# Kernel tuning notes

Hardware: AMD Instinct MI355X
Metric: run time of the kernel (lower is better)

The kernel has to match this reference:

```python
import jax, jax.numpy as jnp
import numpy as np
import math

DIM = 2048
NUM_HEADS = 16
NUM_KV_HEADS = 4
HEAD_DIM = DIM // NUM_HEADS  # 128
KV_DIM = DIM * NUM_KV_HEADS // NUM_HEADS  # 512
B, T = 4, 2048


def setup_inputs() -> dict:
    key = jax.random.key(0)
    ks = jax.random.split(key, 12)
    s = 0.02
    return {
        "x": jax.random.normal(ks[0], (B, T, DIM), dtype=jnp.float32),
        "cos": jax.random.uniform(ks[1], (T, HEAD_DIM // 2), dtype=jnp.float32),
        "sin": jax.random.uniform(ks[2], (T, HEAD_DIM // 2), dtype=jnp.float32),
        "Wq": jax.random.normal(ks[3], (DIM, DIM), dtype=jnp.float32) * s,
        "bq": jnp.zeros((DIM,), dtype=jnp.float32),
        "Wk": jax.random.normal(ks[4], (DIM, KV_DIM), dtype=jnp.float32) * s,
        "bk": jnp.zeros((KV_DIM,), dtype=jnp.float32),
        "Wv": jax.random.normal(ks[5], (DIM, KV_DIM), dtype=jnp.float32) * s,
        "bv": jnp.zeros((KV_DIM,), dtype=jnp.float32),
        "Wo": jax.random.normal(ks[6], (DIM, DIM), dtype=jnp.float32) * s,
        "bo": jnp.zeros((DIM,), dtype=jnp.float32),
    }


def _rope(t, cos, sin):
    # t: [B, H, T, D]; cos/sin: [T, D/2] broadcast over (B, H)
    t1, t2 = t[..., ::2], t[..., 1::2]
    return jnp.concatenate([t1 * cos - t2 * sin, t1 * sin + t2 * cos], axis=-1)


def reference(x, cos, sin, Wq, bq, Wk, bk, Wv, bv, Wo, bo):
    Bx, Tx, C = x.shape
    q = (x @ Wq + bq).reshape(Bx, Tx, NUM_HEADS, HEAD_DIM).transpose(0, 2, 1, 3)
    k = (x @ Wk + bk).reshape(Bx, Tx, NUM_KV_HEADS, HEAD_DIM).transpose(0, 2, 1, 3)
    v = (x @ Wv + bv).reshape(Bx, Tx, NUM_KV_HEADS, HEAD_DIM).transpose(0, 2, 1, 3)
    rep = NUM_HEADS // NUM_KV_HEADS
    k = jnp.repeat(k, rep, axis=1)
    v = jnp.repeat(v, rep, axis=1)
    q = _rope(q, cos, sin)
    k = _rope(k, cos, sin)
    scores = jnp.einsum("bhqd,bhkd->bhqk", q, k) / math.sqrt(HEAD_DIM)
    attn = jax.nn.softmax(scores, axis=-1)
    out = jnp.einsum("bhqk,bhkd->bhqd", attn, v)
    out = out.transpose(0, 2, 1, 3).reshape(Bx, Tx, C)
    return out @ Wo + bo
```

## Files before the change

kernel.cpp:

```cpp
#include <hip/hip_runtime.h>

typedef unsigned short u16;
using bf16x8 = __attribute__((ext_vector_type(8))) short;
using u16x8  = __attribute__((ext_vector_type(8))) unsigned short;
using f32x4  = __attribute__((ext_vector_type(4))) float;
using u32x2  = __attribute__((ext_vector_type(2))) unsigned int;

__device__ __forceinline__ u16 f2bf(float f) {
  unsigned u = __float_as_uint(f);
  u += 0x7FFFu + ((u >> 16) & 1u);
  return (u16)(u >> 16);
}

__device__ __forceinline__ void gload_lds16(const void* g, void* l) {
  __builtin_amdgcn_global_load_lds(
      (const __attribute__((address_space(1))) unsigned int*)g,
      (__attribute__((address_space(3))) unsigned int*)l, 16, 0, 0);
}

__global__ __launch_bounds__(256) void k_cvt(const float* __restrict__ src,
                                             u16* __restrict__ dst) {
  size_t i = (size_t)blockIdx.x * 256 + threadIdx.x;
  const float4* s4 = (const float4*)src;
  float4 a = s4[i * 2], b = s4[i * 2 + 1];
  u16x8 r;
  r[0] = f2bf(a.x); r[1] = f2bf(a.y); r[2] = f2bf(a.z); r[3] = f2bf(a.w);
  r[4] = f2bf(b.x); r[5] = f2bf(b.y); r[6] = f2bf(b.z); r[7] = f2bf(b.w);
  *(u16x8*)(dst + i * 8) = r;
}

__global__ void k_transpose_cvt(const float* __restrict__ src, u16* __restrict__ dst,
                                int R, int C) {
  __shared__ float tile[32][33];
  int bx = blockIdx.x * 32, by = blockIdx.y * 32;
  int tx = threadIdx.x, ty = threadIdx.y;
#pragma unroll
  for (int j = 0; j < 4; ++j)
    tile[ty + j * 8][tx] = src[(size_t)(by + ty + j * 8) * C + bx + tx];
  __syncthreads();
#pragma unroll
  for (int j = 0; j < 4; ++j)
    dst[(size_t)(bx + ty + j * 8) * R + by + tx] = f2bf(tile[tx][ty + j * 8]);
}

__device__ __forceinline__ void gemm_core128(const u16* __restrict__ A,
                                             const u16* __restrict__ Bt, int K,
                                             int m0, int n0, u16* As, u16* Bs,
                                             f32x4 acc[4][4]) {
  const int tid  = threadIdx.x;
  const int lane = tid & 63;
  const int w    = tid >> 6;
  const int wr   = (w >> 1) * 64;
  const int wc   = (w & 1) * 64;
  const int srow = (w << 3) + (lane >> 3);
  const int scol = (lane & 7) << 3;
  const int lm   = lane & 15;
  const int lk   = (lane >> 4) << 3;

  for (int kt = 0; kt < K; kt += 64) {
#pragma unroll
    for (int i = 0; i < 4; ++i) {
      int r = (i << 5) + srow;
      gload_lds16(A  + (size_t)(m0 + r) * K + kt + scol, As + ((i * 4 + w) << 9));
      gload_lds16(Bt + (size_t)(n0 + r) * K + kt + scol, Bs + ((i * 4 + w) << 9));
    }
    __syncthreads();
#pragma unroll
    for (int kk = 0; kk < 64; kk += 32) {
      bf16x8 af[4], bfr[4];
#pragma unroll
      for (int m = 0; m < 4; ++m)
        af[m] = *(const bf16x8*)(As + (wr + m * 16 + lm) * 64 + kk + lk);
#pragma unroll
      for (int n = 0; n < 4; ++n)
        bfr[n] = *(const bf16x8*)(Bs + (wc + n * 16 + lm) * 64 + kk + lk);
#pragma unroll
      for (int m = 0; m < 4; ++m)
#pragma unroll
        for (int n = 0; n < 4; ++n)
          acc[m][n] = __builtin_amdgcn_mfma_f32_16x16x32_bf16(af[m], bfr[n], acc[m][n], 0, 0, 0);
    }
    __syncthreads();
  }
}

__global__ __launch_bounds__(256, 2) void k_qkv(
    const u16* __restrict__ xb, const u16* __restrict__ wT,
    const float* __restrict__ bq, const float* __restrict__ bk, const float* __restrict__ bv,
    const float* __restrict__ cosb, const float* __restrict__ sinb,
    u16* __restrict__ qbuf, u16* __restrict__ kbuf, u16* __restrict__ vbufT) {
  __shared__ u16 As[128 * 64], Bs[128 * 64];
  const int mt = blockIdx.x, nt = blockIdx.y;
  f32x4 acc[4][4];
#pragma unroll
  for (int m = 0; m < 4; ++m)
#pragma unroll
    for (int n = 0; n < 4; ++n) { f32x4 z = {0.f, 0.f, 0.f, 0.f}; acc[m][n] = z; }
  gemm_core128(xb, wT, 2048, mt * 128, nt * 128, As, Bs, acc);

  const int lane = threadIdx.x & 63, w = threadIdx.x >> 6;
  const int row0 = mt * 128 + (w >> 1) * 64 + ((lane >> 4) << 2);
  const int col0 = nt * 128 + (w & 1) * 64 + (lane & 15);
  const float qscale = 0.12751744f;

#pragma unroll
  for (int m = 0; m < 4; ++m) {
#pragma unroll
    for (int n = 0; n < 4; ++n) {
      const int gc = col0 + n * 16;
#pragma unroll
      for (int i = 0; i < 4; ++i) {
        const int gr = row0 + m * 16 + i;
        const int b = gr >> 11, t = gr & 2047;
        float v = acc[m][n][i];
        if (nt < 16) {
          int h = gc >> 7, d = gc & 127;
          float val = v + bq[gc];
          float part = __shfl_xor(val, 1);
          int ir = d >> 1;
          float c = cosb[t * 64 + ir], s = sinb[t * 64 + ir];
          float outv; int dd;
          if (d & 1) { outv = part * s + val * c; dd = ir + 64; }
          else       { outv = val * c - part * s; dd = ir; }
          qbuf[(((size_t)(b * 16 + h) * 2048 + t) << 7) + dd] = f2bf(outv * qscale);
        } else if (nt < 20) {
          int g2 = gc - 2048;
          int kvh = g2 >> 7, d = g2 & 127;
          float val = v + bk[g2];
          float part = __shfl_xor(val, 1);
          int ir = d >> 1;
          float c = cosb[t * 64 + ir], s = sinb[t * 64 + ir];
          float outv; int dd;
          if (d & 1) { outv = part * s + val * c; dd = ir + 64; }
          else       { outv = val * c - part * s; dd = ir; }
          kbuf[(((size_t)(b * 4 + kvh) * 2048 + t) << 7) + dd] = f2bf(outv);
        } else {
          int g2 = gc - 2560;
          int kvh = g2 >> 7, d = g2 & 127;
          float val = v + bv[g2];
          vbufT[((size_t)((b * 4 + kvh) * 128 + d)) * 2048 + t] = f2bf(val);
        }
      }
    }
  }
}

__global__ __launch_bounds__(128, 2) void k_attn(const u16* __restrict__ qbuf,
                                                 const u16* __restrict__ kbuf,
                                                 const u16* __restrict__ vbufT,
                                                 u16* __restrict__ ob) {
  __shared__ u16 Ks[64 * 128];
  __shared__ u16 Vs[128 * 64];
  __shared__ u16 Ps[64 * 64];

  const int f = blockIdx.x;
  const int x = f & 7, mm = f >> 3;
  const int g = x * 2 + (mm >> 7);
  const int mem = mm & 127;
  const int b = g >> 2, kvh = g & 3;
  const int h = kvh * 4 + (mem >> 5);
  const int qt = mem & 31;

  const int tid = threadIdx.x, lane = tid & 63, w = tid >> 6;
  const int lm = lane & 15, lg = lane >> 4;

  const u16* qb = qbuf + ((size_t)((b * 16 + h) * 2048 + qt * 64)) * 128;
  const u16* kb = kbuf + ((size_t)(b * 4 + kvh) * 2048) * 128;
  const u16* vb = vbufT + ((size_t)(b * 4 + kvh) * 128) * 2048;

  bf16x8 qf[2][4];
#pragma unroll
  for (int st = 0; st < 2; ++st)
#pragma unroll
    for (int dc = 0; dc < 4; ++dc)
      qf[st][dc] = *(const bf16x8*)(qb + (size_t)(w * 32 + st * 16 + lm) * 128 + dc * 32 + (lg << 3));

  f32x4 o[2][8];
#pragma unroll
  for (int st = 0; st < 2; ++st)
#pragma unroll
    for (int dn = 0; dn < 8; ++dn) { f32x4 z = {0.f, 0.f, 0.f, 0.f}; o[st][dn] = z; }
  float lsum[2] = {0.f, 0.f};

  for (int kt = 0; kt < 2048; kt += 64) {
#pragma unroll
    for (int j = 0; j < 8; ++j) {
      int seg = j * 2 + w;
      int cK = seg * 64 + lane;
      int rK = cK >> 4, ccK = cK & 15;
      gload_lds16(kb + (size_t)(kt + rK) * 128 + ((ccK ^ (rK & 7)) << 3), Ks + (seg << 9));
      int dV = seg * 8 + (lane >> 3), ccV = lane & 7;
      gload_lds16(vb + (size_t)dV * 2048 + kt + ((ccV ^ (dV & 7)) << 3), Vs + (seg << 9));
    }
    __syncthreads();

#pragma unroll
    for (int kg = 0; kg < 4; ++kg) {
      const int krow = kg * 16 + lm;
      bf16x8 kf[4];
#pragma unroll
      for (int dc = 0; dc < 4; ++dc)
        kf[dc] = *(const bf16x8*)(Ks + krow * 128 + (((dc * 4 + lg) ^ (krow & 7)) << 3));
      f32x4 s0 = {0.f, 0.f, 0.f, 0.f}, s1 = {0.f, 0.f, 0.f, 0.f};
#pragma unroll
      for (int dc = 0; dc < 4; ++dc) {
        s0 = __builtin_amdgcn_mfma_f32_16x16x32_bf16(kf[dc], qf[0][dc], s0, 0, 0, 0);
        s1 = __builtin_amdgcn_mfma_f32_16x16x32_bf16(kf[dc], qf[1][dc], s1, 0, 0, 0);
      }
#pragma unroll
      for (int st = 0; st < 2; ++st) {
        f32x4 sv = st ? s1 : s0;
        float p0 = __builtin_amdgcn_exp2f(sv[0]);
        float p1 = __builtin_amdgcn_exp2f(sv[1]);
        float p2 = __builtin_amdgcn_exp2f(sv[2]);
        float p3 = __builtin_amdgcn_exp2f(sv[3]);
        lsum[st] += (p0 + p1) + (p2 + p3);
        unsigned lo = (unsigned)f2bf(p0) | ((unsigned)f2bf(p1) << 16);
        unsigned hi = (unsigned)f2bf(p2) | ((unsigned)f2bf(p3) << 16);
        const int q = w * 32 + st * 16 + lm;
        const int chunk = kg * 2 + (lg >> 1);
        u16* dst = Ps + q * 64 + ((chunk ^ (q & 7)) << 3) + ((lg & 1) << 2);
        u32x2 pk; pk[0] = lo; pk[1] = hi;
        *reinterpret_cast<u32x2*>(dst) = pk;
      }
    }

#pragma unroll
    for (int kstep = 0; kstep < 2; ++kstep) {
      bf16x8 pf[2];
#pragma unroll
      for (int st = 0; st < 2; ++st) {
        const int q = w * 32 + st * 16 + lm;
        pf[st] = *(const bf16x8*)(Ps + q * 64 + (((kstep * 4 + lg) ^ (q & 7)) << 3));
      }
#pragma unroll
      for (int dn = 0; dn < 8; ++dn) {
        const int d = dn * 16 + lm;
        bf16x8 vf = *(const bf16x8*)(Vs + d * 64 + (((kstep * 4 + lg) ^ (d & 7)) << 3));
        o[0][dn] = __builtin_amdgcn_mfma_f32_16x16x32_bf16(pf[0], vf, o[0][dn], 0, 0, 0);
        o[1][dn] = __builtin_amdgcn_mfma_f32_16x16x32_bf16(pf[1], vf, o[1][dn], 0, 0, 0);
      }
    }
    __syncthreads();
  }

#pragma unroll
  for (int st = 0; st < 2; ++st) {
    float L = lsum[st];
    L += __shfl_xor(L, 16);
    L += __shfl_xor(L, 32);
#pragma unroll
    for (int i = 0; i < 4; ++i) {
      float inv = 1.0f / __shfl(L, lg * 4 + i);
      int t = qt * 64 + w * 32 + st * 16 + lg * 4 + i;
#pragma unroll
      for (int dn = 0; dn < 8; ++dn) {
        int d = dn * 16 + lm;
        ob[((size_t)(b * 2048 + t)) * 2048 + h * 128 + d] = f2bf(o[st][dn][i] * inv);
      }
    }
  }
}

__global__ __launch_bounds__(256, 2) void k_oproj(const u16* __restrict__ ab,
                                                  const u16* __restrict__ woT,
                                                  const float* __restrict__ bo,
                                                  float* __restrict__ out) {
  __shared__ u16 As[128 * 64], Bs[128 * 64];
  const int mt = blockIdx.x, nt = blockIdx.y;
  f32x4 acc[4][4];
#pragma unroll
  for (int m = 0; m < 4; ++m)
#pragma unroll
    for (int n = 0; n < 4; ++n) { f32x4 z = {0.f, 0.f, 0.f, 0.f}; acc[m][n] = z; }
  gemm_core128(ab, woT, 2048, mt * 128, nt * 128, As, Bs, acc);

  const int lane = threadIdx.x & 63, w = threadIdx.x >> 6;
  const int row0 = mt * 128 + (w >> 1) * 64 + ((lane >> 4) << 2);
  const int col0 = nt * 128 + (w & 1) * 64 + (lane & 15);
#pragma unroll
  for (int m = 0; m < 4; ++m)
#pragma unroll
    for (int n = 0; n < 4; ++n) {
      const int gc = col0 + n * 16;
      const float bias = bo[gc];
#pragma unroll
      for (int i = 0; i < 4; ++i) {
        const int gr = row0 + m * 16 + i;
        out[(size_t)gr * 2048 + gc] = acc[m][n][i] + bias;
      }
    }
}

extern "C" void kernel_launch(void* const* d_in, const int* in_sizes, int n_in,
                              void* d_out, int out_size, void* d_ws, size_t ws_size,
                              hipStream_t stream) {
  const float* x    = (const float*)d_in[0];
  const float* cosb = (const float*)d_in[1];
  const float* sinb = (const float*)d_in[2];
  const float* Wq   = (const float*)d_in[3];
  const float* bq   = (const float*)d_in[4];
  const float* Wk   = (const float*)d_in[5];
  const float* bk   = (const float*)d_in[6];
  const float* Wv   = (const float*)d_in[7];
  const float* bv   = (const float*)d_in[8];
  const float* Wo   = (const float*)d_in[9];
  const float* bo   = (const float*)d_in[10];
  float* out = (float*)d_out;

  u16* ws    = (u16*)d_ws;
  u16* xb    = ws;
  u16* wqkvT = xb    + (size_t)8192 * 2048;
  u16* woT   = wqkvT + (size_t)3072 * 2048;
  u16* qbuf  = woT   + (size_t)2048 * 2048;
  u16* kbuf  = qbuf  + (size_t)8192 * 2048;
  u16* vbufT = kbuf  + (size_t)8192 * 512;
  u16* attn  = xb;

  k_cvt<<<8192, 256, 0, stream>>>(x, xb);
  dim3 tb(32, 8);
  k_transpose_cvt<<<dim3(64, 64), tb, 0, stream>>>(Wq, wqkvT, 2048, 2048);
  k_transpose_cvt<<<dim3(16, 64), tb, 0, stream>>>(Wk, wqkvT + (size_t)2048 * 2048, 2048, 512);
  k_transpose_cvt<<<dim3(16, 64), tb, 0, stream>>>(Wv, wqkvT + (size_t)2560 * 2048, 2048, 512);
  k_transpose_cvt<<<dim3(64, 64), tb, 0, stream>>>(Wo, woT, 2048, 2048);

  k_qkv<<<dim3(64, 24), 256, 0, stream>>>(xb, wqkvT, bq, bk, bv, cosb, sinb, qbuf, kbuf, vbufT);
  k_attn<<<2048, 128, 0, stream>>>(qbuf, kbuf, vbufT, attn);
  k_oproj<<<dim3(64, 16), 256, 0, stream>>>(attn, woT, bo, out);
}
```

Measured before the change: 436.0 us.

## Double-buffer K/V tiles in attention with 256-thread blocks and packed bf16 cvt

The attention kernel now uses 256-thread blocks covering 128 query rows, which halves the grid and shares each staged K/V tile across twice as many queries. K/V tiles are double-buffered in LDS, with the next tile prefetched by async global-to-LDS loads while the current one is computed, using manual vmcnt waits and barriers. MFMA sections are wrapped in setprio, and the bf16 packing of probabilities uses the hardware v_cvt_pk_bf16_f32 instruction. LDS use rises to about 80KB per block, which may cut occupancy, and the manual waitcnt scheduling is fragile.

```diff
diff --git a/kernel.cpp b/kernel.cpp
--- a/kernel.cpp
+++ b/kernel.cpp
@@ -10,6 +10,12 @@
   unsigned u = __float_as_uint(f);
   u += 0x7FFFu + ((u >> 16) & 1u);
   return (u16)(u >> 16);
+}
+
+__device__ __forceinline__ unsigned cvt_pk_bf16(float lo, float hi) {
+  unsigned r;
+  asm("v_cvt_pk_bf16_f32 %0, %1, %2" : "=v"(r) : "v"(lo), "v"(hi));
+  return r;
 }
 
 __device__ __forceinline__ void gload_lds16(const void* g, void* l) {
@@ -145,26 +151,26 @@
   }
 }
 
-__global__ __launch_bounds__(128, 2) void k_attn(const u16* __restrict__ qbuf,
+__global__ __launch_bounds__(256, 2) void k_attn(const u16* __restrict__ qbuf,
                                                  const u16* __restrict__ kbuf,
                                                  const u16* __restrict__ vbufT,
                                                  u16* __restrict__ ob) {
-  __shared__ u16 Ks[64 * 128];
-  __shared__ u16 Vs[128 * 64];
-  __shared__ u16 Ps[64 * 64];
+  __shared__ u16 Ks[2][64 * 128];
+  __shared__ u16 Vs[2][128 * 64];
+  __shared__ u16 Ps[128 * 64];
 
   const int f = blockIdx.x;
   const int x = f & 7, mm = f >> 3;
-  const int g = x * 2 + (mm >> 7);
-  const int mem = mm & 127;
+  const int g = x * 2 + (mm >> 6);
+  const int mem = mm & 63;
   const int b = g >> 2, kvh = g & 3;
-  const int h = kvh * 4 + (mem >> 5);
-  const int qt = mem & 31;
+  const int h = kvh * 4 + (mem >> 4);
+  const int qt = mem & 15;
 
   const int tid = threadIdx.x, lane = tid & 63, w = tid >> 6;
   const int lm = lane & 15, lg = lane >> 4;
 
-  const u16* qb = qbuf + ((size_t)((b * 16 + h) * 2048 + qt * 64)) * 128;
+  const u16* qb = qbuf + ((size_t)((b * 16 + h) * 2048 + qt * 128)) * 128;
   const u16* kb = kbuf + ((size_t)(b * 4 + kvh) * 2048) * 128;
   const u16* vb = vbufT + ((size_t)(b * 4 + kvh) * 128) * 2048;
 
@@ -182,17 +188,32 @@
     for (int dn = 0; dn < 8; ++dn) { f32x4 z = {0.f, 0.f, 0.f, 0.f}; o[st][dn] = z; }
   float lsum[2] = {0.f, 0.f};
 
-  for (int kt = 0; kt < 2048; kt += 64) {
-#pragma unroll
-    for (int j = 0; j < 8; ++j) {
-      int seg = j * 2 + w;
-      int cK = seg * 64 + lane;
+  auto stage = [&](int buf, int kt) {
+#pragma unroll
+    for (int j = 0; j < 4; ++j) {
+      int s  = w * 4 + j;
+      int cK = s * 64 + lane;
       int rK = cK >> 4, ccK = cK & 15;
-      gload_lds16(kb + (size_t)(kt + rK) * 128 + ((ccK ^ (rK & 7)) << 3), Ks + (seg << 9));
-      int dV = seg * 8 + (lane >> 3), ccV = lane & 7;
-      gload_lds16(vb + (size_t)dV * 2048 + kt + ((ccV ^ (dV & 7)) << 3), Vs + (seg << 9));
-    }
-    __syncthreads();
+      gload_lds16(kb + (size_t)(kt + rK) * 128 + ((ccK ^ (rK & 7)) << 3), &Ks[buf][s << 9]);
+      int dV = s * 8 + (lane >> 3), ccV = lane & 7;
+      gload_lds16(vb + (size_t)dV * 2048 + kt + ((ccV ^ (dV & 7)) << 3), &Vs[buf][s << 9]);
+    }
+  };
+
+  stage(0, 0);
+  int cur = 0;
+  for (int t = 0; t < 32; ++t) {
+    const int kt = t << 6;
+    if (t < 31) {
+      stage(cur ^ 1, kt + 64);
+      asm volatile("s_waitcnt vmcnt(8)" ::: "memory");
+    } else {
+      asm volatile("s_waitcnt vmcnt(0)" ::: "memory");
+    }
+    __builtin_amdgcn_s_barrier();
+    __builtin_amdgcn_sched_barrier(0);
+    const u16* KsC = Ks[cur];
+    const u16* VsC = Vs[cur];
 
 #pragma unroll
     for (int kg = 0; kg < 4; ++kg) {
@@ -200,13 +221,15 @@
       bf16x8 kf[4];
 #pragma unroll
       for (int dc = 0; dc < 4; ++dc)
-        kf[dc] = *(const bf16x8*)(Ks + krow * 128 + (((dc * 4 + lg) ^ (krow & 7)) << 3));
+        kf[dc] = *(const bf16x8*)(KsC + krow * 128 + (((dc * 4 + lg) ^ (krow & 7)) << 3));
       f32x4 s0 = {0.f, 0.f, 0.f, 0.f}, s1 = {0.f, 0.f, 0.f, 0.f};
+      __builtin_amdgcn_s_setprio(1);
 #pragma unroll
       for (int dc = 0; dc < 4; ++dc) {
         s0 = __builtin_amdgcn_mfma_f32_16x16x32_bf16(kf[dc], qf[0][dc], s0, 0, 0, 0);
         s1 = __builtin_amdgcn_mfma_f32_16x16x32_bf16(kf[dc], qf[1][dc], s1, 0, 0, 0);
       }
+      __builtin_amdgcn_s_setprio(0);
 #pragma unroll
       for (int st = 0; st < 2; ++st) {
         f32x4 sv = st ? s1 : s0;
@@ -215,12 +238,12 @@
         float p2 = __builtin_amdgcn_exp2f(sv[2]);
         float p3 = __builtin_amdgcn_exp2f(sv[3]);
         lsum[st] += (p0 + p1) + (p2 + p3);
-        unsigned lo = (unsigned)f2bf(p0) | ((unsigned)f2bf(p1) << 16);
-        unsigned hi = (unsigned)f2bf(p2) | ((unsigned)f2bf(p3) << 16);
+        u32x2 pk;
+        pk[0] = cvt_pk_bf16(p0, p1);
+        pk[1] = cvt_pk_bf16(p2, p3);
         const int q = w * 32 + st * 16 + lm;
         const int chunk = kg * 2 + (lg >> 1);
         u16* dst = Ps + q * 64 + ((chunk ^ (q & 7)) << 3) + ((lg & 1) << 2);
-        u32x2 pk; pk[0] = lo; pk[1] = hi;
         *reinterpret_cast<u32x2*>(dst) = pk;
       }
     }
@@ -233,15 +256,19 @@
         const int q = w * 32 + st * 16 + lm;
         pf[st] = *(const bf16x8*)(Ps + q * 64 + (((kstep * 4 + lg) ^ (q & 7)) << 3));
       }
+      __builtin_amdgcn_s_setprio(1);
 #pragma unroll
       for (int dn = 0; dn < 8; ++dn) {
         const int d = dn * 16 + lm;
-        bf16x8 vf = *(const bf16x8*)(Vs + d * 64 + (((kstep * 4 + lg) ^ (d & 7)) << 3));
+        bf16x8 vf = *(const bf16x8*)(VsC + d * 64 + (((kstep * 4 + lg) ^ (d & 7)) << 3));
         o[0][dn] = __builtin_amdgcn_mfma_f32_16x16x32_bf16(pf[0], vf, o[0][dn], 0, 0, 0);
         o[1][dn] = __builtin_amdgcn_mfma_f32_16x16x32_bf16(pf[1], vf, o[1][dn], 0, 0, 0);
       }
-    }
-    __syncthreads();
+      __builtin_amdgcn_s_setprio(0);
+    }
+    __builtin_amdgcn_sched_barrier(0);
+    __builtin_amdgcn_s_barrier();
+    cur ^= 1;
   }
 
 #pragma unroll
@@ -252,7 +279,7 @@
 #pragma unroll
     for (int i = 0; i < 4; ++i) {
       float inv = 1.0f / __shfl(L, lg * 4 + i);
-      int t = qt * 64 + w * 32 + st * 16 + lg * 4 + i;
+      int t = qt * 128 + w * 32 + st * 16 + lg * 4 + i;
 #pragma unroll
       for (int dn = 0; dn < 8; ++dn) {
         int d = dn * 16 + lm;
@@ -325,6 +352,6 @@
   k_transpose_cvt<<<dim3(64, 64), tb, 0, stream>>>(Wo, woT, 2048, 2048);
 
   k_qkv<<<dim3(64, 24), 256, 0, stream>>>(xb, wqkvT, bq, bk, bv, cosb, sinb, qbuf, kbuf, vbufT);
-  k_attn<<<2048, 128, 0, stream>>>(qbuf, kbuf, vbufT, attn);
+  k_attn<<<1024, 256, 0, stream>>>(qbuf, kbuf, vbufT, attn);
   k_oproj<<<dim3(64, 16), 256, 0, stream>>>(attn, woT, bo, out);
 }
```

After: 404.4 us. 1.08x faster.
